# Optimization experiments

Measured on AMD Instinct MI355X. Metric: run time of the kernel, lower is better.

Reference implementation:

```python
import jax, jax.numpy as jnp
import numpy as np
import math

EPS = 1e-6

def _rmsnorm(x, w):
    var = jnp.mean(x * x, axis=-1, keepdims=True)
    return x * jax.lax.rsqrt(var + EPS) * w

def _rotary(x, cos, sin):
    d = x.shape[-1] // 2
    x1, x2 = x[..., :d], x[..., d:]
    return jnp.concatenate([x1 * cos - x2 * sin, x2 * cos + x1 * sin], axis=-1)

def _conv1x1(x, w):
    # x: (B, C, 1, S), w: (O, C) -> (B, O, 1, S)
    return jnp.einsum('bcls,oc->bols', x, w)

def setup_inputs() -> dict:
    key = jax.random.key(0)
    ks = jax.random.split(key, 12)
    B, H, KVH, D, S, T, HID = 8, 16, 2, 128, 16, 8192, 2048
    return {
        'x': jax.random.normal(ks[0], (B, HID, 1, S), jnp.float32),
        'cos': jax.random.uniform(ks[1], (1, 1, S, D // 2), jnp.float32),
        'sin': jax.random.uniform(ks[2], (1, 1, S, D // 2), jnp.float32),
        'kv_cache_k': jax.random.normal(ks[3], (B, KVH, T, D), jnp.float32),
        'kv_cache_v': jax.random.normal(ks[4], (B, KVH, T, D), jnp.float32),
        'position': 4096,
        'mask': jnp.zeros((1, 1, S, T), jnp.float32),
        'wq': jax.random.normal(ks[5], (H * D, HID), jnp.float32) * 0.02,
        'wk': jax.random.normal(ks[6], (KVH * D, HID), jnp.float32) * 0.02,
        'wv': jax.random.normal(ks[7], (KVH * D, HID), jnp.float32) * 0.02,
        'wo': jax.random.normal(ks[8], (HID, H * D), jnp.float32) * 0.02,
        'q_norm_w': jnp.ones((D,), jnp.float32),
        'k_norm_w': jnp.ones((D,), jnp.float32),
    }

def reference(x, cos, sin, kv_cache_k, kv_cache_v, position, mask,
              wq, wk, wv, wo, q_norm_w, k_norm_w):
    B, S = x.shape[0], x.shape[3]
    D = q_norm_w.shape[0]
    H = wq.shape[0] // D
    KVH = wk.shape[0] // D
    G = H // KVH  # GQA group size

    # projections (1x1 conv == channel matmul), then (B, h, S, D)
    q = _conv1x1(x, wq)[:, :, 0, :].reshape(B, H, D, S).transpose(0, 1, 3, 2)
    k = _conv1x1(x, wk)[:, :, 0, :].reshape(B, KVH, D, S).transpose(0, 1, 3, 2)
    v = _conv1x1(x, wv)[:, :, 0, :].reshape(B, KVH, D, S).transpose(0, 1, 3, 2)

    q = _rotary(_rmsnorm(q, q_norm_w), cos, sin)
    k = _rotary(_rmsnorm(k, k_norm_w), cos, sin)

    # scatter new k/v into cache at `position`
    new_k = jax.lax.dynamic_update_slice(kv_cache_k, k, (0, 0, position, 0))
    new_v = jax.lax.dynamic_update_slice(kv_cache_v, v, (0, 0, position, 0))

    # GQA: fold q heads into (kv_head, group) so K/V need no repeat_interleave
    scale = 1.0 / math.sqrt(D)
    qg = q.reshape(B, KVH, G, S, D)
    attn = jnp.einsum('bkgsd,bktd->bkgst', qg, new_k) * scale
    attn = attn + mask[:, :, None, :, :]  # (1,1,S,T) -> broadcast over groups
    probs = jax.nn.softmax(attn, axis=-1)
    out = jnp.einsum('bkgst,bktd->bkgsd', probs, new_v).reshape(B, H, S, D)

    # back to (B, H*D, 1, S) and output projection
    out = out.transpose(0, 1, 3, 2).reshape(B, H * D, 1, S)
    out = _conv1x1(out, wo)
    return out, new_k, new_v
```

## Files before the change

### kernel.cpp

```cpp
#include <hip/hip_runtime.h>
#include <cstdint>
#include <cstddef>


typedef __attribute__((ext_vector_type(8))) short bf16x8;
typedef __attribute__((ext_vector_type(4))) float f32x4;
typedef unsigned short u16;
typedef unsigned int u32;

#define MFMA16(a, b, c) __builtin_amdgcn_mfma_f32_16x16x32_bf16(a, b, c, 0, 0, 0)

static __device__ __forceinline__ u16 f2bf(float f) {
  u32 u = __float_as_uint(f);
  u += 0x7FFFu + ((u >> 16) & 1u);
  return (u16)(u >> 16);
}
static __device__ __forceinline__ float bf2f(u16 u) {
  return __uint_as_float(((u32)u) << 16);
}
static __device__ __forceinline__ u32 pk2(float a, float b) {
  return (u32)f2bf(a) | ((u32)f2bf(b) << 16);
}

__global__ __launch_bounds__(256) void transpose_x(const float* __restrict__ x,
                                                   u16* __restrict__ Xt) {
  int id = blockIdx.x * 256 + threadIdx.x;
  int b = id >> 13, c = (id >> 2) & 2047, s4 = id & 3;
  float4 v = *(const float4*)(x + ((size_t)(b * 2048 + c)) * 16 + s4 * 4);
  size_t base = (size_t)(b * 16 + s4 * 4) * 2048 + c;
  Xt[base]        = f2bf(v.x);
  Xt[base + 2048] = f2bf(v.y);
  Xt[base + 4096] = f2bf(v.z);
  Xt[base + 6144] = f2bf(v.w);
}

template <int MODE>
__global__ __launch_bounds__(256) void gemm16(const float* __restrict__ w0,
                                              const float* __restrict__ w1,
                                              const float* __restrict__ w2,
                                              const u16* __restrict__ Bt,
                                              float* __restrict__ outp) {
  __shared__ __align__(16) u16 sW[16 * 256];
  const int tid = threadIdx.x, lane = tid & 63, w = tid >> 6;
  const int q = lane >> 4, n = lane & 15;
  const int m0 = blockIdx.x * 16;
  const int kp = blockIdx.y;
  const int kbase = kp * 256;
  const float* wbase;
  if (MODE == 0) {
    if (m0 < 2048)      wbase = w0 + (size_t)m0 * 2048;
    else if (m0 < 2304) wbase = w1 + (size_t)(m0 - 2048) * 2048;
    else                wbase = w2 + (size_t)(m0 - 2304) * 2048;
  } else {
    wbase = w0 + (size_t)m0 * 2048;
  }
  {
    int m = tid >> 4, s16 = tid & 15;
    const float* src = wbase + (size_t)m * 2048 + kbase + s16 * 16;
    float4 a = *(const float4*)(src);
    float4 b = *(const float4*)(src + 4);
    float4 c = *(const float4*)(src + 8);
    float4 d = *(const float4*)(src + 12);
    uint4 u0 = {pk2(a.x, a.y), pk2(a.z, a.w), pk2(b.x, b.y), pk2(b.z, b.w)};
    uint4 u1 = {pk2(c.x, c.y), pk2(c.z, c.w), pk2(d.x, d.y), pk2(d.z, d.w)};
    int G0 = 2 * s16;
    *(uint4*)&sW[m * 256 + ((G0 + m) & 31) * 8]     = u0;
    *(uint4*)&sW[m * 256 + ((G0 + 1 + m) & 31) * 8] = u1;
  }
  bf16x8 bfr[2][8];
#pragma unroll
  for (int e = 0; e < 2; ++e) {
    int j = 32 * w + 16 * e + n;
    const u16* bp = Bt + (size_t)j * 2048 + kbase + q * 8;
#pragma unroll
    for (int ks = 0; ks < 8; ++ks) bfr[e][ks] = *(const bf16x8*)(bp + ks * 32);
  }
  __syncthreads();
  f32x4 acc0 = {0.f, 0.f, 0.f, 0.f}, acc1 = acc0;
#pragma unroll
  for (int ks = 0; ks < 8; ++ks) {
    bf16x8 af = *(const bf16x8*)&sW[n * 256 + (((4 * ks + q) + n) & 31) * 8];
    acc0 = MFMA16(af, bfr[0][ks], acc0);
    acc1 = MFMA16(af, bfr[1][ks], acc1);
  }
#pragma unroll
  for (int e = 0; e < 2; ++e) {
    f32x4 a = e ? acc1 : acc0;
    int j = 32 * w + 16 * e + n;
    if (MODE == 0) {
      *(f32x4*)&outp[(size_t)kp * 327680 + (size_t)j * 2560 + m0 + 4 * q] = a;
    } else {
#pragma unroll
      for (int reg = 0; reg < 4; ++reg) {
        int m = m0 + 4 * q + reg;
        outp[(size_t)kp * 262144 + (size_t)(j >> 4) * 32768 + m * 16 + (j & 15)] =
            a[reg];
      }
    }
  }
}

__global__ __launch_bounds__(256) void reduce_out(const float* __restrict__ part,
                                                  float* __restrict__ out) {
  int i = blockIdx.x * 256 + threadIdx.x;
  f32x4 acc = {0.f, 0.f, 0.f, 0.f};
#pragma unroll
  for (int p = 0; p < 8; ++p)
    acc += *(const f32x4*)(part + (size_t)p * 262144 + (size_t)i * 4);
  *(f32x4*)(out + (size_t)i * 4) = acc;
}

__global__ __launch_bounds__(256) void norm_rot(
    const float* __restrict__ qkvp, const float* __restrict__ cosb,
    const float* __restrict__ sinb, const float* __restrict__ qw,
    const float* __restrict__ kw,
    u16* __restrict__ Qa, float* __restrict__ knew, float* __restrict__ vnew) {
  const int wid = blockIdx.x * 4 + (threadIdx.x >> 6);
  const int lane = threadIdx.x & 63;
  const float SCALE = 0.08838834764831845f;
  if (wid < 2048) {
    int b = wid >> 8, h = (wid >> 4) & 15, s = wid & 15;
    int j = b * 16 + s;
    const float* row = qkvp + (size_t)j * 2560 + h * 128;
    float v1 = 0.f, v2 = 0.f;
#pragma unroll
    for (int p = 0; p < 8; ++p) {
      v1 += row[(size_t)p * 327680 + lane];
      v2 += row[(size_t)p * 327680 + lane + 64];
    }
    float ss = v1 * v1 + v2 * v2;
#pragma unroll
    for (int o = 32; o > 0; o >>= 1) ss += __shfl_xor(ss, o, 64);
    float rr = rsqrtf(ss * (1.0f / 128.0f) + 1e-6f);
    float n1 = v1 * rr * qw[lane];
    float n2 = v2 * rr * qw[lane + 64];
    float c = cosb[s * 64 + lane], sn = sinb[s * 64 + lane];
    u16* dst = Qa + (size_t)((b * 16 + h) * 16 + s) * 128;
    dst[lane]      = f2bf((n1 * c - n2 * sn) * SCALE);
    dst[lane + 64] = f2bf((n2 * c + n1 * sn) * SCALE);
  } else if (wid < 2304) {
    int idx = wid - 2048;
    int b = idx >> 5, kvh = (idx >> 4) & 1, s = idx & 15;
    int j = b * 16 + s;
    const float* row = qkvp + (size_t)j * 2560 + 2048 + kvh * 128;
    float v1 = 0.f, v2 = 0.f;
#pragma unroll
    for (int p = 0; p < 8; ++p) {
      v1 += row[(size_t)p * 327680 + lane];
      v2 += row[(size_t)p * 327680 + lane + 64];
    }
    float ss = v1 * v1 + v2 * v2;
#pragma unroll
    for (int o = 32; o > 0; o >>= 1) ss += __shfl_xor(ss, o, 64);
    float rr = rsqrtf(ss * (1.0f / 128.0f) + 1e-6f);
    float n1 = v1 * rr * kw[lane];
    float n2 = v2 * rr * kw[lane + 64];
    float c = cosb[s * 64 + lane], sn = sinb[s * 64 + lane];
    float* dst = knew + (size_t)((b * 2 + kvh) * 16 + s) * 128;
    dst[lane]      = n1 * c - n2 * sn;
    dst[lane + 64] = n2 * c + n1 * sn;
  } else {
    int idx = wid - 2304;
    int b = idx >> 5, kvh = (idx >> 4) & 1, s = idx & 15;
    int j = b * 16 + s;
    const float* row = qkvp + (size_t)j * 2560 + 2304 + kvh * 128;
    float v1 = 0.f, v2 = 0.f;
#pragma unroll
    for (int p = 0; p < 8; ++p) {
      v1 += row[(size_t)p * 327680 + lane];
      v2 += row[(size_t)p * 327680 + lane + 64];
    }
    float* dst = vnew + (size_t)((b * 2 + kvh) * 16 + s) * 128;
    dst[lane]      = v1;
    dst[lane + 64] = v2;
  }
}

__global__ __launch_bounds__(256, 2) void attn(
    const u16* __restrict__ Qa, const float* __restrict__ kcache,
    const float* __restrict__ vcache, const float* __restrict__ knew,
    const float* __restrict__ vnew, const int* __restrict__ posp,
    const float* __restrict__ mask, float* __restrict__ outk,
    float* __restrict__ outv, u16* __restrict__ Opart,
    float* __restrict__ Mpart, float* __restrict__ Lpart) {
  __shared__ __align__(16) u16 sQ[16384];
  __shared__ __align__(16) u16 sP[8192];
  __shared__ __align__(16) u16 sVt[8192];

  const int tid = threadIdx.x, lane = tid & 63, w = tid >> 6;
  const int q = lane >> 4, n = lane & 15;
  const int bid = blockIdx.x;
  const int bk = bid >> 5, chunk = bid & 31;
  const int b = bk >> 1, kvh = bk & 1;
  const int pos = *posp;

  for (int i = tid; i < 2048; i += 256) {
    int r = i >> 4, g = i & 15;
    int h = kvh * 8 + (r >> 4), s = r & 15;
    uint4 v = *(const uint4*)(Qa + (size_t)((b * 16 + h) * 16 + s) * 128 + g * 8);
    *(uint4*)&sQ[r * 128 + ((g + r) & 15) * 8] = v;
  }
  __syncthreads();
  bf16x8 qf[2][4];
#pragma unroll
  for (int e = 0; e < 2; ++e) {
    int r = 32 * w + 16 * e + n;
#pragma unroll
    for (int ks = 0; ks < 4; ++ks)
      qf[e][ks] = *(const bf16x8*)&sQ[r * 128 + (((4 * ks + q) + r) & 15) * 8];
  }
  __syncthreads();

  bf16x8 idE = {0, 0, 0, 0, 0, 0, 0, 0}, idO = idE;
  {
    const short one = (short)0x3F80;
    int tq = n >> 3, te = n & 7;
#pragma unroll
    for (int e = 0; e < 8; ++e) {
      if (q == tq && e == te) idE[e] = one;
      if (q == tq + 2 && e == te) idO[e] = one;
    }
  }

  float m_old[2] = {-INFINITY, -INFINITY}, l_old[2] = {0.f, 0.f};
  f32x4 oacc[2][8];
#pragma unroll
  for (int e = 0; e < 2; ++e)
#pragma unroll
    for (int nt = 0; nt < 8; ++nt) oacc[e][nt] = (f32x4){0.f, 0.f, 0.f, 0.f};

  for (int tile = 0; tile < 4; ++tile) {
    const int t0 = chunk * 256 + tile * 64;
    for (int i = tid; i < 2048; i += 256) {
      int isV = i >> 10;
      int tl = (i >> 4) & 63, g = i & 15;
      int tg = t0 + tl;
      const float* src;
      float* dst;
      if (!isV) {
        src = (tg >= pos && tg < pos + 16)
                  ? (knew + (size_t)(bk * 16 + (tg - pos)) * 128)
                  : (kcache + ((size_t)bk * 8192 + tg) * 128);
        dst = outk + ((size_t)bk * 8192 + tg) * 128;
      } else {
        src = (tg >= pos && tg < pos + 16)
                  ? (vnew + (size_t)(bk * 16 + (tg - pos)) * 128)
                  : (vcache + ((size_t)bk * 8192 + tg) * 128);
        dst = outv + ((size_t)bk * 8192 + tg) * 128;
      }
      float4 a = *(const float4*)(src + g * 8);
      float4 b2 = *(const float4*)(src + g * 8 + 4);
      *(float4*)(dst + g * 8) = a;
      *(float4*)(dst + g * 8 + 4) = b2;
      uint4 u = {pk2(a.x, a.y), pk2(a.z, a.w), pk2(b2.x, b2.y), pk2(b2.z, b2.w)};
      *(uint4*)&sQ[isV * 8192 + tl * 128 + ((g + tl) & 15) * 8] = u;
    }
    float mv[4][4];
#pragma unroll
    for (int mt = 0; mt < 4; ++mt)
#pragma unroll
      for (int rg = 0; rg < 4; ++rg)
        mv[mt][rg] = mask[(size_t)n * 8192 + t0 + 16 * mt + 4 * q + rg];
    __syncthreads();

    f32x4 sacc[4][2];
#pragma unroll
    for (int mt = 0; mt < 4; ++mt) {
      sacc[mt][0] = (f32x4){0.f, 0.f, 0.f, 0.f};
      sacc[mt][1] = sacc[mt][0];
    }
#pragma unroll
    for (int ks = 0; ks < 4; ++ks) {
#pragma unroll
      for (int mt = 0; mt < 4; ++mt) {
        int trow = 16 * mt + n;
        bf16x8 kf = *(const bf16x8*)&sQ[trow * 128 + (((4 * ks + q) + trow) & 15) * 8];
        sacc[mt][0] = MFMA16(kf, qf[0][ks], sacc[mt][0]);
        sacc[mt][1] = MFMA16(kf, qf[1][ks], sacc[mt][1]);
      }
    }

#pragma unroll
    for (int mtv = 0; mtv < 4; ++mtv) {
      int trow = 16 * mtv + n;
      bf16x8 vfr = *(const bf16x8*)&sQ[8192 + trow * 128 + (((4 * w + q) + trow) & 15) * 8];
      f32x4 z = {0.f, 0.f, 0.f, 0.f};
      f32x4 d0 = MFMA16(vfr, idE, z);
      f32x4 d1 = MFMA16(vfr, idO, z);
      int G = 2 * mtv + (q >> 1), off = 4 * (q & 1);
      int dp0 = 32 * w + n, dp1 = dp0 + 16;
      uint2 u0 = {pk2(d0[0], d0[1]), pk2(d0[2], d0[3])};
      uint2 u1 = {pk2(d1[0], d1[1]), pk2(d1[2], d1[3])};
      *(uint2*)&sVt[dp0 * 64 + ((G + dp0) & 7) * 8 + off] = u0;
      *(uint2*)&sVt[dp1 * 64 + ((G + dp1) & 7) * 8 + off] = u1;
    }

    float al[2];
#pragma unroll
    for (int e = 0; e < 2; ++e) {
      float sv[4][4];
      float mx = -INFINITY;
#pragma unroll
      for (int mt = 0; mt < 4; ++mt)
#pragma unroll
        for (int rg = 0; rg < 4; ++rg) {
          float v = sacc[mt][e][rg] + mv[mt][rg];
          sv[mt][rg] = v;
          mx = fmaxf(mx, v);
        }
      mx = fmaxf(mx, __shfl_xor(mx, 16));
      mx = fmaxf(mx, __shfl_xor(mx, 32));
      float mn = fmaxf(m_old[e], mx);
      al[e] = __expf(m_old[e] - mn);
      float ts = 0.f;
      int r = 32 * w + 16 * e + n;
#pragma unroll
      for (int mt = 0; mt < 4; ++mt) {
        float p0 = __expf(sv[mt][0] - mn), p1 = __expf(sv[mt][1] - mn);
        float p2 = __expf(sv[mt][2] - mn), p3 = __expf(sv[mt][3] - mn);
        ts += (p0 + p1) + (p2 + p3);
        uint2 up = {pk2(p0, p1), pk2(p2, p3)};
        int G = 2 * mt + (q >> 1), off = 4 * (q & 1);
        *(uint2*)&sP[r * 64 + ((G + r) & 7) * 8 + off] = up;
      }
      ts += __shfl_xor(ts, 16);
      ts += __shfl_xor(ts, 32);
      l_old[e] = l_old[e] * al[e] + ts;
      m_old[e] = mn;
    }
    __syncthreads();

#pragma unroll
    for (int e = 0; e < 2; ++e) {
      float an[4];
#pragma unroll
      for (int rg = 0; rg < 4; ++rg) an[rg] = __shfl(al[e], 4 * q + rg);
#pragma unroll
      for (int nt = 0; nt < 8; ++nt)
#pragma unroll
        for (int rg = 0; rg < 4; ++rg) oacc[e][nt][rg] *= an[rg];
    }
    bf16x8 Pf[2][2];
#pragma unroll
    for (int e = 0; e < 2; ++e) {
      int r = 32 * w + 16 * e + n;
#pragma unroll
      for (int ks = 0; ks < 2; ++ks)
        Pf[e][ks] = *(const bf16x8*)&sP[r * 64 + (((4 * ks + q) + r) & 7) * 8];
    }
#pragma unroll
    for (int nt = 0; nt < 8; ++nt) {
      int d = 16 * nt + n;
#pragma unroll
      for (int ks = 0; ks < 2; ++ks) {
        bf16x8 vf = *(const bf16x8*)&sVt[d * 64 + (((4 * ks + q) + d) & 7) * 8];
        oacc[0][nt] = MFMA16(Pf[0][ks], vf, oacc[0][nt]);
        oacc[1][nt] = MFMA16(Pf[1][ks], vf, oacc[1][nt]);
      }
    }
    __syncthreads();
  }

#pragma unroll
  for (int e = 0; e < 2; ++e)
#pragma unroll
    for (int nt = 0; nt < 8; ++nt) {
      int d = 16 * nt + n;
      int r0 = 32 * w + 16 * e + 4 * q;
      int G = r0 >> 3, off = 4 * (q & 1);
      uint2 u = {pk2(oacc[e][nt][0], oacc[e][nt][1]),
                 pk2(oacc[e][nt][2], oacc[e][nt][3])};
      *(uint2*)&sQ[d * 128 + ((G + d) & 15) * 8 + off] = u;
    }
  if (q == 0) {
#pragma unroll
    for (int e = 0; e < 2; ++e) {
      int r = 32 * w + 16 * e + n;
      Mpart[(size_t)bid * 128 + r] = m_old[e];
      Lpart[(size_t)bid * 128 + r] = l_old[e];
    }
  }
  __syncthreads();
  for (int i = tid; i < 2048; i += 256) {
    int d = i >> 4, g = i & 15;
    uint4 v = *(const uint4*)&sQ[d * 128 + ((g + d) & 15) * 8];
    *(uint4*)(Opart + (size_t)bid * 16384 + d * 128 + g * 8) = v;
  }
}

__global__ __launch_bounds__(256) void combine(const u16* __restrict__ Opart,
                                               const float* __restrict__ Mp,
                                               const float* __restrict__ Lp,
                                               u16* __restrict__ A2t) {
  __shared__ float wgt[32 * 128];
  const int tid = threadIdx.x;
  const int bk = blockIdx.x, dgrp = blockIdx.y;
  if (tid < 128) {
    int r = tid;
    float mc[32], M = -INFINITY;
#pragma unroll
    for (int c = 0; c < 32; ++c) {
      mc[c] = Mp[(size_t)(bk * 32 + c) * 128 + r];
      M = fmaxf(M, mc[c]);
    }
    float L = 0.f, wv[32];
#pragma unroll
    for (int c = 0; c < 32; ++c) {
      wv[c] = __expf(mc[c] - M);
      L += wv[c] * Lp[(size_t)(bk * 32 + c) * 128 + r];
    }
    float inv = 1.0f / L;
#pragma unroll
    for (int c = 0; c < 32; ++c) wgt[c * 128 + r] = wv[c] * inv;
  }
  __syncthreads();
  int r = tid & 127, dd = tid >> 7;
  int b = bk >> 1, kvh = bk & 1;
  int h = kvh * 8 + (r >> 4), s = r & 15;
  size_t arow = (size_t)(b * 16 + s) * 2048 + h * 128;
  float o[4] = {0.f, 0.f, 0.f, 0.f};
#pragma unroll
  for (int c = 0; c < 32; ++c) {
    float wv = wgt[c * 128 + r];
    size_t base = ((size_t)(bk * 32 + c) * 128) * 128 + r;
#pragma unroll
    for (int di = 0; di < 4; ++di) {
      int d = dgrp * 8 + dd + 2 * di;
      o[di] += wv * bf2f(Opart[base + (size_t)d * 128]);
    }
  }
#pragma unroll
  for (int di = 0; di < 4; ++di) {
    int d = dgrp * 8 + dd + 2 * di;
    A2t[arow + d] = f2bf(o[di]);
  }
}

extern "C" void kernel_launch(void* const* d_in, const int* in_sizes, int n_in,
                              void* d_out, int out_size, void* d_ws, size_t ws_size,
                              hipStream_t stream) {
  const float* x    = (const float*)d_in[0];
  const float* cosb = (const float*)d_in[1];
  const float* sinb = (const float*)d_in[2];
  const float* kc   = (const float*)d_in[3];
  const float* vc   = (const float*)d_in[4];
  const int*   posp = (const int*)d_in[5];
  const float* mask = (const float*)d_in[6];
  const float* wq   = (const float*)d_in[7];
  const float* wk   = (const float*)d_in[8];
  const float* wv   = (const float*)d_in[9];
  const float* wo   = (const float*)d_in[10];
  const float* qw   = (const float*)d_in[11];
  const float* kw   = (const float*)d_in[12];

  float* out  = (float*)d_out;
  float* outk = out + 262144;
  float* outv = outk + 16777216;

  float* ws     = (float*)d_ws;
  float* ws_A   = ws;
  float* ws_knew = ws + 4194304;
  float* ws_vnew = ws + 4227072;
  u16*   ws_Qa   = (u16*)(ws + 4259840);
  u16*   ws_Xt   = (u16*)(ws + 4390912);
  u16*   ws_A2t  = (u16*)(ws + 4521984);
  float* ws_M    = ws + 4653056;
  float* ws_L    = ws + 4718592;

  float* ws_qkvp = ws_A;
  u16*   ws_O    = (u16*)ws_A;
  float* ws_op   = ws_A;

  transpose_x<<<256, 256, 0, stream>>>(x, ws_Xt);
  gemm16<0><<<dim3(160, 8), 256, 0, stream>>>(wq, wk, wv, ws_Xt, ws_qkvp);
  norm_rot<<<640, 256, 0, stream>>>(ws_qkvp, cosb, sinb, qw, kw,
                                    ws_Qa, ws_knew, ws_vnew);
  attn<<<512, 256, 0, stream>>>(ws_Qa, kc, vc, ws_knew, ws_vnew, posp, mask,
                                outk, outv, ws_O, ws_M, ws_L);
  combine<<<dim3(16, 16), 256, 0, stream>>>(ws_O, ws_M, ws_L, ws_A2t);
  gemm16<1><<<dim3(128, 8), 256, 0, stream>>>(wo, wo, wo, ws_A2t, ws_op);
  reduce_out<<<256, 256, 0, stream>>>(ws_op, out);
}
```

Measured before the change: 332.4 us.

## Split KV cache update into a standalone copy kernel before attention

Moves the scatter of new K/V rows and the full cache copy out of the attention kernel into a dedicated vectorized cache_copy kernel. Attention then reads K/V from the freshly written output caches instead of doing copy and conversion together. This simplifies the attention inner load loop and gives the copy a fully parallel grid. The cost is an extra pass over the caches, since the outputs are written and then read back by attention, which adds memory traffic.

```diff
diff --git a/kernel.cpp b/kernel.cpp
--- a/kernel.cpp
+++ b/kernel.cpp
@@ -176,13 +176,39 @@
   }
 }
 
+__global__ __launch_bounds__(256) void cache_copy(
+    const float* __restrict__ kcache, const float* __restrict__ vcache,
+    const float* __restrict__ knew, const float* __restrict__ vnew,
+    const int* __restrict__ posp,
+    float* __restrict__ outk, float* __restrict__ outv) {
+  const int pos = *posp;
+  const float4* kc4 = (const float4*)kcache;
+  const float4* vc4 = (const float4*)vcache;
+  const float4* kn4 = (const float4*)knew;
+  const float4* vn4 = (const float4*)vnew;
+  float4* ok4 = (float4*)outk;
+  float4* ov4 = (float4*)outv;
+  size_t t = (size_t)blockIdx.x * 256 + threadIdx.x;
+#pragma unroll
+  for (int it = 0; it < 4; ++it) {
+    size_t i = t + (size_t)it * 1048576;
+    int row = (int)(i >> 5), d4 = (int)(i & 31);
+    int bk = row >> 13, tr = row & 8191;
+    int sub = tr - pos;
+    bool isNew = (u32)sub < 16u;
+    size_t nidx = (size_t)(bk * 16 + (sub & 15)) * 32 + d4;
+    float4 kv = isNew ? kn4[nidx] : kc4[i];
+    ok4[i] = kv;
+    float4 vv = isNew ? vn4[nidx] : vc4[i];
+    ov4[i] = vv;
+  }
+}
+
 __global__ __launch_bounds__(256, 2) void attn(
-    const u16* __restrict__ Qa, const float* __restrict__ kcache,
-    const float* __restrict__ vcache, const float* __restrict__ knew,
-    const float* __restrict__ vnew, const int* __restrict__ posp,
-    const float* __restrict__ mask, float* __restrict__ outk,
-    float* __restrict__ outv, u16* __restrict__ Opart,
-    float* __restrict__ Mpart, float* __restrict__ Lpart) {
+    const u16* __restrict__ Qa, const float* __restrict__ Kc,
+    const float* __restrict__ Vc, const float* __restrict__ mask,
+    u16* __restrict__ Opart, float* __restrict__ Mpart,
+    float* __restrict__ Lpart) {
   __shared__ __align__(16) u16 sQ[16384];
   __shared__ __align__(16) u16 sP[8192];
   __shared__ __align__(16) u16 sVt[8192];
@@ -192,7 +218,6 @@
   const int bid = blockIdx.x;
   const int bk = bid >> 5, chunk = bid & 31;
   const int b = bk >> 1, kvh = bk & 1;
-  const int pos = *posp;
 
   for (int i = tid; i < 2048; i += 256) {
     int r = i >> 4, g = i & 15;
@@ -235,23 +260,9 @@
       int isV = i >> 10;
       int tl = (i >> 4) & 63, g = i & 15;
       int tg = t0 + tl;
-      const float* src;
-      float* dst;
-      if (!isV) {
-        src = (tg >= pos && tg < pos + 16)
-                  ? (knew + (size_t)(bk * 16 + (tg - pos)) * 128)
-                  : (kcache + ((size_t)bk * 8192 + tg) * 128);
-        dst = outk + ((size_t)bk * 8192 + tg) * 128;
-      } else {
-        src = (tg >= pos && tg < pos + 16)
-                  ? (vnew + (size_t)(bk * 16 + (tg - pos)) * 128)
-                  : (vcache + ((size_t)bk * 8192 + tg) * 128);
-        dst = outv + ((size_t)bk * 8192 + tg) * 128;
-      }
-      float4 a = *(const float4*)(src + g * 8);
-      float4 b2 = *(const float4*)(src + g * 8 + 4);
-      *(float4*)(dst + g * 8) = a;
-      *(float4*)(dst + g * 8 + 4) = b2;
+      const float* src = (isV ? Vc : Kc) + ((size_t)bk * 8192 + tg) * 128 + g * 8;
+      float4 a = *(const float4*)(src);
+      float4 b2 = *(const float4*)(src + 4);
       uint4 u = {pk2(a.x, a.y), pk2(a.z, a.w), pk2(b2.x, b2.y), pk2(b2.z, b2.w)};
       *(uint4*)&sQ[isV * 8192 + tl * 128 + ((g + tl) & 15) * 8] = u;
     }
@@ -475,8 +486,9 @@
   gemm16<0><<<dim3(160, 8), 256, 0, stream>>>(wq, wk, wv, ws_Xt, ws_qkvp);
   norm_rot<<<640, 256, 0, stream>>>(ws_qkvp, cosb, sinb, qw, kw,
                                     ws_Qa, ws_knew, ws_vnew);
-  attn<<<512, 256, 0, stream>>>(ws_Qa, kc, vc, ws_knew, ws_vnew, posp, mask,
-                                outk, outv, ws_O, ws_M, ws_L);
+  cache_copy<<<4096, 256, 0, stream>>>(kc, vc, ws_knew, ws_vnew, posp,
+                                       outk, outv);
+  attn<<<512, 256, 0, stream>>>(ws_Qa, outk, outv, mask, ws_O, ws_M, ws_L);
   combine<<<dim3(16, 16), 256, 0, stream>>>(ws_O, ws_M, ws_L, ws_A2t);
   gemm16<1><<<dim3(128, 8), 256, 0, stream>>>(wo, wo, wo, ws_A2t, ws_op);
   reduce_out<<<256, 256, 0, stream>>>(ws_op, out);
```

Measured after the change: 365.0 us. 1.1x slower.
